# Kernel tuning notes

Hardware: AMD Instinct MI355X
Metric: run time of the kernel (lower is better)

Reference implementation:

```python
import jax, jax.numpy as jnp
import numpy as np

# WeightOnlyInt8Linear forward: out = (x @ W_int8.astype(x.dtype).T) * scales
# NOTE: the original torch forward has a bug: when bias is not None it returns
# pre_bias (bias is never added), and when bias is None it would crash.
# Faithful math for a runnable configuration (bias=True) is therefore just
# the scaled matmul without bias.

IN_FEATURES = 4096
OUT_FEATURES = 16384
M = 256  # tokens


def setup_inputs() -> dict:
    key = jax.random.key(0)
    k1, k2, k3 = jax.random.split(key, 3)
    x = jax.random.normal(k1, (M, IN_FEATURES), dtype=jnp.float32)
    # int8 quantized weights in [-128, 127]
    weight = jax.random.randint(k2, (OUT_FEATURES, IN_FEATURES), -128, 128, dtype=jnp.int8)
    # per-output-channel dequant scales (positive, small)
    scales = jax.random.uniform(k3, (OUT_FEATURES,), dtype=jnp.float32, minval=0.001, maxval=0.02)
    return {"input": x, "weight": weight, "scales": scales}


def reference(input, weight, scales):
    # weight.to(input): upcast int8 -> activation dtype, then dense GEMM, then per-channel scale
    w = weight.astype(input.dtype)                      # [out, in]
    pre_bias = jnp.einsum('mk,nk->mn', input, w)        # [M, out]
    return pre_bias * scales                            # broadcast over out_features
```

## Files before the change

kernel.cpp:

```cpp
#include <hip/hip_runtime.h>
#include <stdint.h>

#define M_TOK 256
#define N_OUT 16384
#define K_IN  4096
#define BM 128
#define BN 64
#define BK 64
#define NSTEPS (K_IN / BK)

#define AS1 __attribute__((address_space(1)))
#define AS3 __attribute__((address_space(3)))

typedef short v8s __attribute__((ext_vector_type(8)));
typedef float v16f __attribute__((ext_vector_type(16)));
typedef int   v4i __attribute__((ext_vector_type(4)));
typedef unsigned int uint;

__device__ __forceinline__ unsigned short rne_bf16(float f) {
  uint u = __float_as_uint(f);
  uint r = u + 0x7FFFu + ((u >> 16) & 1u);
  return (unsigned short)(r >> 16);
}
__device__ __forceinline__ float bfbits_to_f(uint h) {
  return __uint_as_float(h << 16);
}
__device__ __forceinline__ uint pack_bf16(float a, float b) {
  return (__float_as_uint(a) >> 16) | (__float_as_uint(b) & 0xffff0000u);
}

__global__ __launch_bounds__(256) void cast_kernel(
    const float* __restrict__ x, unsigned short* __restrict__ xhi,
    unsigned short* __restrict__ xlo) {
  const int i = (blockIdx.x * 256 + threadIdx.x) * 4;
  const float4 f = *(const float4*)(x + i);
  float fs[4] = {f.x, f.y, f.z, f.w};
  unsigned short h[4], l[4];
#pragma unroll
  for (int j = 0; j < 4; ++j) {
    h[j] = rne_bf16(fs[j]);
    l[j] = rne_bf16(fs[j] - bfbits_to_f(h[j]));
  }
  *(ushort4*)(xhi + i) = make_ushort4(h[0], h[1], h[2], h[3]);
  *(ushort4*)(xlo + i) = make_ushort4(l[0], l[1], l[2], l[3]);
}

__global__ __launch_bounds__(512, 4) void gemm_kernel(
    const unsigned short* __restrict__ xhi, const unsigned short* __restrict__ xlo,
    const void* __restrict__ wraw, const float* __restrict__ scales,
    float* __restrict__ out) {
  __shared__ alignas(16) unsigned char smem[40960];
  const int tid = threadIdx.x;
  const int lane = tid & 63;
  const int wid = tid >> 6;

  const int* wi = (const int*)wraw;
  const signed char* wb = (const signed char*)wraw;
  bool is32 = true;
#pragma unroll
  for (int i = 0; i < 16; ++i) {
    const int v = wi[i];
    is32 = is32 && (v >= -128) && (v <= 127);
  }

  const int bid = blockIdx.x;
  const int logical = (bid & 7) * 64 + (bid >> 3);
  const int mb = logical & 1;
  const int nb = logical >> 1;
  const int m0 = mb * BM;
  const int n0 = nb * BN;

  const unsigned short* xsrc[4];
  uint xdst[4];
#pragma unroll
  for (int j = 0; j < 4; ++j) {
    const int s = wid * 4 + j;
    const int r = s * 4 + (lane >> 4);
    const int c = (lane & 15) ^ (r & 15);
    xsrc[j] = (c >= 8 ? xlo : xhi) + (size_t)(m0 + r) * K_IN + (size_t)((c & 7) * 8);
    xdst[j] = (uint)(s * 1024);
  }

  const int wrow = tid >> 3, wc = tid & 7;
  const int* w32base = wi + (size_t)(n0 + wrow) * K_IN + (size_t)(wc * 8);
  const signed char* w8base = wb + (size_t)(n0 + wrow) * K_IN + (size_t)(wc * 8);
  const uint wq = (uint)(wrow >> 1);
  const uint wchunk = (uint)((wrow & 1) * 8 + wc);
  const uint waddr = 32768u + wq * 256u + ((wchunk ^ (wq & 15u)) << 4);

  const int l31 = lane & 31, hi5 = lane >> 5;
  const int wm = (wid & 3) * 32;
  const int wn = (wid >> 2) * 32;
  const uint abase = (uint)((wm + l31) * 256);
  const uint ax = (uint)((wm + l31) & 15);
  const int wr = wn + l31;
  const uint bq = (uint)(wr >> 1);
  const uint bbase = 32768u + bq * 256u;
  const uint bsel = (uint)((wr & 1) * 8);
  const uint bx = bq & 15u;

  v16f acc = {};
  v4i wt0, wt1;

  auto stage_x = [&](int s) {
#pragma unroll
    for (int j = 0; j < 4; ++j)
      __builtin_amdgcn_global_load_lds(
          (const AS1 void*)(xsrc[j] + (size_t)s * BK),
          (AS3 void*)(smem + xdst[j]), 16, 0, 0);
  };
  auto load_w = [&](int s) {
    if (is32) {
      wt0 = *(const v4i*)(w32base + (size_t)s * BK);
      wt1 = *(const v4i*)(w32base + (size_t)s * BK + 4);
    } else {
      const uint2 u = *(const uint2*)(w8base + (size_t)s * BK);
      wt0.x = (int)u.x; wt0.y = (int)u.y;
    }
  };
  auto conv_w = [&]() {
    uint d[4];
    if (is32) {
      d[0] = pack_bf16((float)wt0.x, (float)wt0.y);
      d[1] = pack_bf16((float)wt0.z, (float)wt0.w);
      d[2] = pack_bf16((float)wt1.x, (float)wt1.y);
      d[3] = pack_bf16((float)wt1.z, (float)wt1.w);
    } else {
      const signed char* bs = (const signed char*)&wt0;
#pragma unroll
      for (int p = 0; p < 4; ++p)
        d[p] = pack_bf16((float)bs[2 * p], (float)bs[2 * p + 1]);
    }
    v4i wv; wv.x = (int)d[0]; wv.y = (int)d[1]; wv.z = (int)d[2]; wv.w = (int)d[3];
    *(v4i*)(smem + waddr) = wv;
  };

  stage_x(0);
  load_w(0);

  for (int t = 0; t < NSTEPS; ++t) {
    conv_w();
    __syncthreads();

    if (t + 1 < NSTEPS) load_w(t + 1);

#pragma unroll
    for (int kc = 0; kc < 4; ++kc) {
      const uint ch = (uint)(kc * 2 + hi5);
      v8s ah = *(const v8s*)(smem + abase + ((ch ^ ax) << 4));
      v8s al = *(const v8s*)(smem + abase + (((ch + 8u) ^ ax) << 4));
      v8s b  = *(const v8s*)(smem + bbase + (((bsel + ch) ^ bx) << 4));
      acc = __builtin_amdgcn_mfma_f32_32x32x16_bf16(ah, b, acc, 0, 0, 0);
      acc = __builtin_amdgcn_mfma_f32_32x32x16_bf16(al, b, acc, 0, 0, 0);
    }

    __syncthreads();
    if (t + 1 < NSTEPS) stage_x(t + 1);
  }

  const int n = n0 + wn + l31;
  const float scl = scales[n];
#pragma unroll
  for (int reg = 0; reg < 16; ++reg) {
    const int m = m0 + wm + (reg & 3) + 8 * (reg >> 2) + 4 * hi5;
    out[(size_t)m * N_OUT + n] = acc[reg] * scl;
  }
}

__global__ void naive_kernel(const float* __restrict__ x, const void* __restrict__ wraw,
                             const float* __restrict__ scales, float* __restrict__ out) {
  const int* wi = (const int*)wraw;
  bool is32 = true;
  for (int i = 0; i < 16; ++i) { int v = wi[i]; is32 = is32 && v >= -128 && v <= 127; }
  const int idx = blockIdx.x * 256 + threadIdx.x;
  const int m = idx >> 14;
  const int n = idx & (N_OUT - 1);
  const float* xr = x + (size_t)m * K_IN;
  float acc = 0.f;
  if (is32) {
    const int* wr = wi + (size_t)n * K_IN;
    for (int k = 0; k < K_IN; ++k) acc += xr[k] * (float)wr[k];
  } else {
    const signed char* wr = (const signed char*)wraw + (size_t)n * K_IN;
    for (int k = 0; k < K_IN; ++k) acc += xr[k] * (float)wr[k];
  }
  out[idx] = acc * scales[n];
}

extern "C" void kernel_launch(void* const* d_in, const int* in_sizes, int n_in,
                              void* d_out, int out_size, void* d_ws, size_t ws_size,
                              hipStream_t stream) {
  const float* x = (const float*)d_in[0];
  const void* w = d_in[1];
  const float* scales = (const float*)d_in[2];
  float* out = (float*)d_out;
  if (ws_size >= (size_t)4 * 1024 * 1024) {
    unsigned short* xhi = (unsigned short*)d_ws;
    unsigned short* xlo = xhi + (size_t)M_TOK * K_IN;
    cast_kernel<<<(M_TOK * K_IN) / 1024, 256, 0, stream>>>(x, xhi, xlo);
    gemm_kernel<<<512, 512, 0, stream>>>(xhi, xlo, w, scales, out);
  } else {
    naive_kernel<<<(M_TOK * N_OUT) / 256, 256, 0, stream>>>(x, w, scales, out);
  }
}
```

Measured before the change: 407.4 us.

## Split K across waves with direct global activation loads and LDS reduction

Each wave now owns a K-quarter and a 64x64 output subtile computed as 2x2 MFMA fragments. Activations are read straight from global into registers instead of being staged through LDS, and the weight tile is double-buffered in LDS so there is one barrier per step instead of two. Partial accumulators from the four K-groups are combined through LDS in a two-level reduction before scaling and storing. This cuts barrier count and LDS traffic for the activation matrix, at the cost of uncoalesced, latency-exposed global activation loads, more accumulator registers, and a reduction epilogue.

```diff
diff --git a/kernel.cpp b/kernel.cpp
--- a/kernel.cpp
+++ b/kernel.cpp
@@ -9,9 +9,6 @@
 #define BK 64
 #define NSTEPS (K_IN / BK)
 
-#define AS1 __attribute__((address_space(1)))
-#define AS3 __attribute__((address_space(3)))
-
 typedef short v8s __attribute__((ext_vector_type(8)));
 typedef float v16f __attribute__((ext_vector_type(16)));
 typedef int   v4i __attribute__((ext_vector_type(4)));
@@ -49,7 +46,7 @@
     const unsigned short* __restrict__ xhi, const unsigned short* __restrict__ xlo,
     const void* __restrict__ wraw, const float* __restrict__ scales,
     float* __restrict__ out) {
-  __shared__ alignas(16) unsigned char smem[40960];
+  __shared__ alignas(16) unsigned char smem[65536];
   const int tid = threadIdx.x;
   const int lane = tid & 63;
   const int wid = tid >> 6;
@@ -70,55 +67,41 @@
   const int m0 = mb * BM;
   const int n0 = nb * BN;
 
-  const unsigned short* xsrc[4];
-  uint xdst[4];
-#pragma unroll
-  for (int j = 0; j < 4; ++j) {
-    const int s = wid * 4 + j;
-    const int r = s * 4 + (lane >> 4);
-    const int c = (lane & 15) ^ (r & 15);
-    xsrc[j] = (c >= 8 ? xlo : xhi) + (size_t)(m0 + r) * K_IN + (size_t)((c & 7) * 8);
-    xdst[j] = (uint)(s * 1024);
-  }
+  const int mp = wid & 1;
+  const int kq = wid >> 1;
+  const int l31 = lane & 31, hi5 = lane >> 5;
+
+  const size_t xrow = (size_t)(m0 + mp * 64 + l31) * K_IN + (size_t)(kq * 16 + hi5 * 8);
+  const unsigned short* pxh = xhi + xrow;
+  const unsigned short* pxl = xlo + xrow;
 
   const int wrow = tid >> 3, wc = tid & 7;
   const int* w32base = wi + (size_t)(n0 + wrow) * K_IN + (size_t)(wc * 8);
   const signed char* w8base = wb + (size_t)(n0 + wrow) * K_IN + (size_t)(wc * 8);
   const uint wq = (uint)(wrow >> 1);
-  const uint wchunk = (uint)((wrow & 1) * 8 + wc);
-  const uint waddr = 32768u + wq * 256u + ((wchunk ^ (wq & 15u)) << 4);
-
-  const int l31 = lane & 31, hi5 = lane >> 5;
-  const int wm = (wid & 3) * 32;
-  const int wn = (wid >> 2) * 32;
-  const uint abase = (uint)((wm + l31) * 256);
-  const uint ax = (uint)((wm + l31) & 15);
-  const int wr = wn + l31;
-  const uint bq = (uint)(wr >> 1);
-  const uint bbase = 32768u + bq * 256u;
-  const uint bsel = (uint)((wr & 1) * 8);
-  const uint bx = bq & 15u;
-
-  v16f acc = {};
+  const uint waddr = wq * 256u + ((uint)(((wrow & 1) * 8 + wc)) ^ (wq & 15u)) * 16u;
+
+  uint baddr[2];
+#pragma unroll
+  for (int nf = 0; nf < 2; ++nf) {
+    const int wr = nf * 32 + l31;
+    const uint q = (uint)(wr >> 1);
+    baddr[nf] = q * 256u + ((uint)((wr & 1) * 8 + kq * 2 + hi5) ^ (q & 15u)) * 16u;
+  }
+
+  v16f acc[2][2] = {};
   v4i wt0, wt1;
-
-  auto stage_x = [&](int s) {
-#pragma unroll
-    for (int j = 0; j < 4; ++j)
-      __builtin_amdgcn_global_load_lds(
-          (const AS1 void*)(xsrc[j] + (size_t)s * BK),
-          (AS3 void*)(smem + xdst[j]), 16, 0, 0);
-  };
+  uint2 w8t;
+
   auto load_w = [&](int s) {
     if (is32) {
       wt0 = *(const v4i*)(w32base + (size_t)s * BK);
       wt1 = *(const v4i*)(w32base + (size_t)s * BK + 4);
     } else {
-      const uint2 u = *(const uint2*)(w8base + (size_t)s * BK);
-      wt0.x = (int)u.x; wt0.y = (int)u.y;
+      w8t = *(const uint2*)(w8base + (size_t)s * BK);
     }
   };
-  auto conv_w = [&]() {
+  auto conv_w = [&](uint wo) {
     uint d[4];
     if (is32) {
       d[0] = pack_bf16((float)wt0.x, (float)wt0.y);
@@ -126,44 +109,90 @@
       d[2] = pack_bf16((float)wt1.x, (float)wt1.y);
       d[3] = pack_bf16((float)wt1.z, (float)wt1.w);
     } else {
-      const signed char* bs = (const signed char*)&wt0;
+      const signed char* bs = (const signed char*)&w8t;
 #pragma unroll
       for (int p = 0; p < 4; ++p)
         d[p] = pack_bf16((float)bs[2 * p], (float)bs[2 * p + 1]);
     }
     v4i wv; wv.x = (int)d[0]; wv.y = (int)d[1]; wv.z = (int)d[2]; wv.w = (int)d[3];
-    *(v4i*)(smem + waddr) = wv;
-  };
-
-  stage_x(0);
+    *(v4i*)(smem + wo + waddr) = wv;
+  };
+
   load_w(0);
+  conv_w(0u);
+  __syncthreads();
 
   for (int t = 0; t < NSTEPS; ++t) {
-    conv_w();
+    const bool more = (t + 1 < NSTEPS);
+    if (more) load_w(t + 1);
+
+    const uint rb = (uint)(t & 1) * 8192u;
+    const size_t ko = (size_t)t * BK;
+    v8s ah0 = *(const v8s*)(pxh + ko);
+    v8s al0 = *(const v8s*)(pxl + ko);
+    v8s ah1 = *(const v8s*)(pxh + (size_t)32 * K_IN + ko);
+    v8s al1 = *(const v8s*)(pxl + (size_t)32 * K_IN + ko);
+    v8s b0 = *(const v8s*)(smem + rb + baddr[0]);
+    v8s b1 = *(const v8s*)(smem + rb + baddr[1]);
+
+    acc[0][0] = __builtin_amdgcn_mfma_f32_32x32x16_bf16(ah0, b0, acc[0][0], 0, 0, 0);
+    acc[0][1] = __builtin_amdgcn_mfma_f32_32x32x16_bf16(ah0, b1, acc[0][1], 0, 0, 0);
+    acc[1][0] = __builtin_amdgcn_mfma_f32_32x32x16_bf16(ah1, b0, acc[1][0], 0, 0, 0);
+    acc[1][1] = __builtin_amdgcn_mfma_f32_32x32x16_bf16(ah1, b1, acc[1][1], 0, 0, 0);
+    acc[0][0] = __builtin_amdgcn_mfma_f32_32x32x16_bf16(al0, b0, acc[0][0], 0, 0, 0);
+    acc[0][1] = __builtin_amdgcn_mfma_f32_32x32x16_bf16(al0, b1, acc[0][1], 0, 0, 0);
+    acc[1][0] = __builtin_amdgcn_mfma_f32_32x32x16_bf16(al1, b0, acc[1][0], 0, 0, 0);
+    acc[1][1] = __builtin_amdgcn_mfma_f32_32x32x16_bf16(al1, b1, acc[1][1], 0, 0, 0);
+
+    if (more) conv_w(rb ^ 8192u);
     __syncthreads();
-
-    if (t + 1 < NSTEPS) load_w(t + 1);
-
-#pragma unroll
-    for (int kc = 0; kc < 4; ++kc) {
-      const uint ch = (uint)(kc * 2 + hi5);
-      v8s ah = *(const v8s*)(smem + abase + ((ch ^ ax) << 4));
-      v8s al = *(const v8s*)(smem + abase + (((ch + 8u) ^ ax) << 4));
-      v8s b  = *(const v8s*)(smem + bbase + (((bsel + ch) ^ bx) << 4));
-      acc = __builtin_amdgcn_mfma_f32_32x32x16_bf16(ah, b, acc, 0, 0, 0);
-      acc = __builtin_amdgcn_mfma_f32_32x32x16_bf16(al, b, acc, 0, 0, 0);
+  }
+
+  auto dump = [&](int ri) {
+#pragma unroll
+    for (int mf = 0; mf < 2; ++mf)
+#pragma unroll
+      for (int nf = 0; nf < 2; ++nf)
+#pragma unroll
+        for (int q = 0; q < 4; ++q) {
+          float4 v = make_float4(acc[mf][nf][4 * q], acc[mf][nf][4 * q + 1],
+                                 acc[mf][nf][4 * q + 2], acc[mf][nf][4 * q + 3]);
+          *(float4*)(smem + ri * 16384 + (mf * 2 + nf) * 4096 + q * 1024 + lane * 16) = v;
+        }
+  };
+  auto take = [&](int ri) {
+#pragma unroll
+    for (int mf = 0; mf < 2; ++mf)
+#pragma unroll
+      for (int nf = 0; nf < 2; ++nf)
+#pragma unroll
+        for (int q = 0; q < 4; ++q) {
+          float4 v = *(const float4*)(smem + ri * 16384 + (mf * 2 + nf) * 4096 +
+                                      q * 1024 + lane * 16);
+          acc[mf][nf][4 * q] += v.x;  acc[mf][nf][4 * q + 1] += v.y;
+          acc[mf][nf][4 * q + 2] += v.z;  acc[mf][nf][4 * q + 3] += v.w;
+        }
+  };
+  if (kq >= 2) dump(mp * 2 + (kq - 2));
+  __syncthreads();
+  if (kq < 2) take(mp * 2 + kq);
+  __syncthreads();
+  if (kq == 1) dump(mp);
+  __syncthreads();
+  if (kq == 0) {
+    take(mp);
+#pragma unroll
+    for (int nf = 0; nf < 2; ++nf) {
+      const int n = n0 + nf * 32 + l31;
+      const float scl = scales[n];
+#pragma unroll
+      for (int mf = 0; mf < 2; ++mf)
+#pragma unroll
+        for (int reg = 0; reg < 16; ++reg) {
+          const int m = m0 + mp * 64 + mf * 32 + (reg & 3) + 8 * (reg >> 2) + 4 * hi5;
+          out[(size_t)m * N_OUT + n] = acc[mf][nf][reg] * scl;
+        }
     }
-
-    __syncthreads();
-    if (t + 1 < NSTEPS) stage_x(t + 1);
-  }
-
-  const int n = n0 + wn + l31;
-  const float scl = scales[n];
-#pragma unroll
-  for (int reg = 0; reg < 16; ++reg) {
-    const int m = m0 + wm + (reg & 3) + 8 * (reg >> 2) + 4 * hi5;
-    out[(size_t)m * N_OUT + n] = acc[reg] * scl;
   }
 }
 
```

Result: slower. 473.3 us (+16.2%).

## Double-buffer LDS tiles to overlap next-step loads with MFMA compute

Applied to the files above, without the earlier changes.

Doubles shared memory to two ping-pong buffers for the x tile and the converted weight tile. The next step's x async copy and weight global load are issued before the current step's MFMAs, and the weight conversion and store into the other buffer happen after compute, leaving one barrier per iteration instead of two. This hides global load latency behind compute. LDS per block rises to 80KB, which may cut blocks per CU (launch bounds request 4) and so lower occupancy.

```diff
diff --git a/kernel.cpp b/kernel.cpp
--- a/kernel.cpp
+++ b/kernel.cpp
@@ -49,7 +49,7 @@
     const unsigned short* __restrict__ xhi, const unsigned short* __restrict__ xlo,
     const void* __restrict__ wraw, const float* __restrict__ scales,
     float* __restrict__ out) {
-  __shared__ alignas(16) unsigned char smem[40960];
+  __shared__ alignas(16) unsigned char smem[81920];
   const int tid = threadIdx.x;
   const int lane = tid & 63;
   const int wid = tid >> 6;
@@ -86,28 +86,28 @@
   const signed char* w8base = wb + (size_t)(n0 + wrow) * K_IN + (size_t)(wc * 8);
   const uint wq = (uint)(wrow >> 1);
   const uint wchunk = (uint)((wrow & 1) * 8 + wc);
-  const uint waddr = 32768u + wq * 256u + ((wchunk ^ (wq & 15u)) << 4);
+  const uint waddr = wq * 256u + ((wchunk ^ (wq & 15u)) << 4);
 
   const int l31 = lane & 31, hi5 = lane >> 5;
   const int wm = (wid & 3) * 32;
   const int wn = (wid >> 2) * 32;
-  const uint abase = (uint)((wm + l31) * 256);
+  const uint arow = (uint)((wm + l31) * 256);
   const uint ax = (uint)((wm + l31) & 15);
   const int wr = wn + l31;
   const uint bq = (uint)(wr >> 1);
-  const uint bbase = 32768u + bq * 256u;
+  const uint bbase = bq * 256u;
   const uint bsel = (uint)((wr & 1) * 8);
   const uint bx = bq & 15u;
 
   v16f acc = {};
   v4i wt0, wt1;
 
-  auto stage_x = [&](int s) {
+  auto stage_x = [&](int s, uint xb) {
 #pragma unroll
     for (int j = 0; j < 4; ++j)
       __builtin_amdgcn_global_load_lds(
           (const AS1 void*)(xsrc[j] + (size_t)s * BK),
-          (AS3 void*)(smem + xdst[j]), 16, 0, 0);
+          (AS3 void*)(smem + xb + xdst[j]), 16, 0, 0);
   };
   auto load_w = [&](int s) {
     if (is32) {
@@ -118,7 +118,7 @@
       wt0.x = (int)u.x; wt0.y = (int)u.y;
     }
   };
-  auto conv_w = [&]() {
+  auto conv_w = [&](uint wo) {
     uint d[4];
     if (is32) {
       d[0] = pack_bf16((float)wt0.x, (float)wt0.y);
@@ -132,30 +132,36 @@
         d[p] = pack_bf16((float)bs[2 * p], (float)bs[2 * p + 1]);
     }
     v4i wv; wv.x = (int)d[0]; wv.y = (int)d[1]; wv.z = (int)d[2]; wv.w = (int)d[3];
-    *(v4i*)(smem + waddr) = wv;
+    *(v4i*)(smem + wo + waddr) = wv;
   };
 
-  stage_x(0);
+  stage_x(0, 0u);
   load_w(0);
+  conv_w(65536u);
+  __syncthreads();
 
   for (int t = 0; t < NSTEPS; ++t) {
-    conv_w();
-    __syncthreads();
-
-    if (t + 1 < NSTEPS) load_w(t + 1);
+    const uint xb = (uint)(t & 1) * 32768u;
+    const uint wo = 65536u + (uint)(t & 1) * 8192u;
+    const bool more = (t + 1 < NSTEPS);
+    if (more) {
+      stage_x(t + 1, xb ^ 32768u);
+      load_w(t + 1);
+    }
+    __builtin_amdgcn_sched_barrier(0);
 
 #pragma unroll
     for (int kc = 0; kc < 4; ++kc) {
       const uint ch = (uint)(kc * 2 + hi5);
-      v8s ah = *(const v8s*)(smem + abase + ((ch ^ ax) << 4));
-      v8s al = *(const v8s*)(smem + abase + (((ch + 8u) ^ ax) << 4));
-      v8s b  = *(const v8s*)(smem + bbase + (((bsel + ch) ^ bx) << 4));
+      v8s ah = *(const v8s*)(smem + xb + arow + ((ch ^ ax) << 4));
+      v8s al = *(const v8s*)(smem + xb + arow + (((ch + 8u) ^ ax) << 4));
+      v8s b  = *(const v8s*)(smem + wo + bbase + (((bsel + ch) ^ bx) << 4));
       acc = __builtin_amdgcn_mfma_f32_32x32x16_bf16(ah, b, acc, 0, 0, 0);
       acc = __builtin_amdgcn_mfma_f32_32x32x16_bf16(al, b, acc, 0, 0, 0);
     }
 
+    if (more) conv_w(wo ^ 8192u);
     __syncthreads();
-    if (t + 1 < NSTEPS) stage_x(t + 1);
   }
 
   const int n = n0 + wn + l31;
```

Result: no change. 412.8 us (+1.3%).
